# Optimization experiments

Hardware: AMD Instinct MI355X
Metric: run time of the kernel (lower is better)

Reference implementation:

```python
import jax, jax.numpy as jnp
import numpy as np

GROUPS = 8
EPS = 1e-5


def group_norm_dim1(x, gamma, beta):
    # Faithful to torch: GroupNorm treats dim 1 (height) as the channel axis.
    B, H, W, C = x.shape
    xg = x.reshape(B, GROUPS, H // GROUPS, W, C)
    mean = xg.mean(axis=(2, 3, 4), keepdims=True)
    var = xg.var(axis=(2, 3, 4), keepdims=True)
    xn = ((xg - mean) * jax.lax.rsqrt(var + EPS)).reshape(B, H, W, C)
    return xn * gamma[None, :, None, None] + beta[None, :, None, None]


def setup_inputs() -> dict:
    key = jax.random.key(0)
    ks = jax.random.split(key, 8)
    B, H, W, C = 4, 64, 64, 64  # height must equal units for GroupNorm to apply
    s = 1.0 / np.sqrt(C)
    return {
        "x": jax.random.normal(ks[0], (B, H, W, C), dtype=jnp.float32),
        "gamma": jnp.ones((C,), jnp.float32),
        "beta": jnp.zeros((C,), jnp.float32),
        "Wq": jax.random.normal(ks[1], (C, C), jnp.float32) * s,
        "bq": jnp.zeros((C,), jnp.float32),
        "Wk": jax.random.normal(ks[2], (C, C), jnp.float32) * s,
        "bk": jnp.zeros((C,), jnp.float32),
        "Wv": jax.random.normal(ks[3], (C, C), jnp.float32) * s,
        "bv": jnp.zeros((C,), jnp.float32),
        "Wo": jax.random.normal(ks[4], (C, C), jnp.float32) * s,
        "bo": jnp.zeros((C,), jnp.float32),
    }


def reference(x, gamma, beta, Wq, bq, Wk, bk, Wv, bv, Wo, bo):
    B, H, W, C = x.shape
    scale = C ** (-0.5)
    xn = group_norm_dim1(x, gamma, beta)
    q = xn @ Wq + bq
    k = xn @ Wk + bk
    v = xn @ Wv + bv
    # full spatial self-attention: scores [B, H, W, H*W]
    scores = jnp.einsum('bhwc,bijc->bhwij', q, k) * scale
    attn = jax.nn.softmax(scores.reshape(B, H, W, H * W), axis=-1)
    attn = attn.reshape(B, H, W, H, W)
    proj = jnp.einsum('bhwij,bijc->bhwc', attn, v)
    proj = proj @ Wo + bo
    return xn + proj
```

## Files before the change

### kernel.cpp

```cpp
#include <hip/hip_runtime.h>

typedef __bf16 bf16_t;
typedef bf16_t bf16x8 __attribute__((ext_vector_type(8)));
typedef bf16_t bf16x4 __attribute__((ext_vector_type(4)));
typedef short  short4v __attribute__((ext_vector_type(4)));
typedef float  f32x4  __attribute__((ext_vector_type(4)));

#define MFMA32(a, b, c) __builtin_amdgcn_mfma_f32_16x16x32_bf16(a, b, c, 0, 0, 0)
#define MFMA16(a, b, c) __builtin_amdgcn_mfma_f32_16x16x16bf16_1k(a, b, c, 0, 0, 0)

__global__ __launch_bounds__(256) void gn1w_kernel(const float* __restrict__ x,
    float2* __restrict__ partials,
    const float* __restrict__ Wq, const float* __restrict__ Wk,
    const float* __restrict__ Wv, const float* __restrict__ Wo,
    bf16_t* __restrict__ Wt) {
  int blk = blockIdx.x, t = threadIdx.x;
  if (blk >= 256) {
    int idx = (blk - 256) * 256 + t;
    int wsel = idx >> 12, rem = idx & 4095;
    int c = rem >> 6, kk = rem & 63;
    const float* src = (wsel == 0) ? Wq : ((wsel == 1) ? Wk : ((wsel == 2) ? Wv : Wo));
    Wt[idx] = (bf16_t)src[kk * 64 + c];
    return;
  }
  const float4* x4 = (const float4*)x + (size_t)blk * 1024;
  float s = 0.f, sq = 0.f;
  #pragma unroll
  for (int u = 0; u < 4; ++u) {
    float4 v = x4[u * 256 + t];
    s  += v.x + v.y + v.z + v.w;
    sq += v.x * v.x + v.y * v.y + v.z * v.z + v.w * v.w;
  }
  for (int off = 32; off; off >>= 1) {
    s  += __shfl_down(s, off, 64);
    sq += __shfl_down(sq, off, 64);
  }
  __shared__ float2 ps[4];
  if ((t & 63) == 0) ps[t >> 6] = make_float2(s, sq);
  __syncthreads();
  if (t == 0) {
    float S = 0.f, Q = 0.f;
    #pragma unroll
    for (int i = 0; i < 4; ++i) { S += ps[i].x; Q += ps[i].y; }
    partials[blk] = make_float2(S, Q);
  }
}

__global__ __launch_bounds__(256) void gnqkv_kernel(
    const float* __restrict__ x, const float* __restrict__ gamma,
    const float* __restrict__ beta, const float2* __restrict__ parts,
    const bf16_t* __restrict__ Wt,
    const float* __restrict__ bq, const float* __restrict__ bk, const float* __restrict__ bv,
    bf16_t* __restrict__ xnb, bf16_t* __restrict__ qo, bf16_t* __restrict__ ko,
    bf16_t* __restrict__ vo) {
  __shared__ __align__(16) bf16_t xl[4096];
  int blk = blockIdx.x, t = threadIdx.x;
  int grp = blk >> 3;
  float S = 0.f, Q = 0.f;
  #pragma unroll
  for (int i = 0; i < 8; ++i) { float2 p = parts[grp * 8 + i]; S += p.x; Q += p.y; }
  float mean = S * (1.f / 32768.f);
  float rstd = rsqrtf(Q * (1.f / 32768.f) - mean * mean + 1e-5f);
  int h = blk & 63;
  float ga = gamma[h] * rstd;
  float be = beta[h] - mean * ga;
  {
    int r = t >> 2, col0 = (t & 3) * 16;
    const float4* x4 = (const float4*)(x + (size_t)blk * 4096 + r * 64 + col0);
    bf16x8 pk0, pk1;
    float4 v0 = x4[0], v1 = x4[1], v2 = x4[2], v3 = x4[3];
    pk0[0] = (bf16_t)(v0.x * ga + be); pk0[1] = (bf16_t)(v0.y * ga + be);
    pk0[2] = (bf16_t)(v0.z * ga + be); pk0[3] = (bf16_t)(v0.w * ga + be);
    pk0[4] = (bf16_t)(v1.x * ga + be); pk0[5] = (bf16_t)(v1.y * ga + be);
    pk0[6] = (bf16_t)(v1.z * ga + be); pk0[7] = (bf16_t)(v1.w * ga + be);
    pk1[0] = (bf16_t)(v2.x * ga + be); pk1[1] = (bf16_t)(v2.y * ga + be);
    pk1[2] = (bf16_t)(v2.z * ga + be); pk1[3] = (bf16_t)(v2.w * ga + be);
    pk1[4] = (bf16_t)(v3.x * ga + be); pk1[5] = (bf16_t)(v3.y * ga + be);
    pk1[6] = (bf16_t)(v3.z * ga + be); pk1[7] = (bf16_t)(v3.w * ga + be);
    *(bf16x8*)&xnb[(size_t)blk * 4096 + r * 64 + col0]     = pk0;
    *(bf16x8*)&xnb[(size_t)blk * 4096 + r * 64 + col0 + 8] = pk1;
    int sw = r & 7, j0 = (t & 3) * 2;
    *(bf16x8*)&xl[r * 64 + ((j0 ^ sw) << 3)]       = pk0;
    *(bf16x8*)&xl[r * 64 + (((j0 + 1) ^ sw) << 3)] = pk1;
  }
  __syncthreads();
  int w = t >> 6, lane = t & 63, quad = lane >> 4, l16 = lane & 15;
  int rl = w * 16 + l16, sw2 = rl & 7;
  bf16x8 a0 = *(const bf16x8*)&xl[rl * 64 + ((quad ^ sw2) << 3)];
  bf16x8 a1 = *(const bf16x8*)&xl[rl * 64 + (((quad + 4) ^ sw2) << 3)];
  int m0 = blk * 64 + w * 16;
  int bi = m0 >> 12;
  f32x4 zero = {0.f, 0.f, 0.f, 0.f};
  const float QSCALE = 0.125f * 1.44269504088896340736f;
  #pragma unroll
  for (int outk = 0; outk < 3; ++outk) {
    const bf16_t* wt = Wt + outk * 4096;
    const float* bias = (outk == 0) ? bq : ((outk == 1) ? bk : bv);
    #pragma unroll
    for (int nt = 0; nt < 4; ++nt) {
      int col = nt * 16 + l16;
      bf16x8 b0 = *(const bf16x8*)&wt[col * 64 + quad * 8];
      bf16x8 b1 = *(const bf16x8*)&wt[col * 64 + 32 + quad * 8];
      f32x4 acc = MFMA32(a0, b0, zero);
      acc = MFMA32(a1, b1, acc);
      float bb = bias[col];
      if (outk == 2) {
        bf16x4 pk;
        #pragma unroll
        for (int r = 0; r < 4; ++r) pk[r] = (bf16_t)(acc[r] + bb);
        *(bf16x4*)&vo[(size_t)bi * 262144 + (size_t)(blk & 63) * 4096
                      + (size_t)col * 64 + w * 16 + quad * 4] = pk;
      } else {
        #pragma unroll
        for (int r = 0; r < 4; ++r) {
          int m = m0 + quad * 4 + r;
          float v = acc[r] + bb;
          if (outk == 0) qo[(size_t)m * 64 + col] = (bf16_t)(v * QSCALE);
          else           ko[(size_t)m * 64 + col] = (bf16_t)v;
        }
      }
    }
  }
}

__global__ __launch_bounds__(128) void flash_kernel(
    const bf16_t* __restrict__ q, const bf16_t* __restrict__ k,
    const bf16_t* __restrict__ vp, bf16_t* __restrict__ Opb, float* __restrict__ ml) {
  __shared__ __align__(16) bf16_t Kb[2][4096];
  __shared__ __align__(16) bf16_t Vb[2][4096];
  int t = threadIdx.x;
  int w = t >> 6, lane = t & 63, quad = lane >> 4, l16 = lane & 15;
  int qb = blockIdx.x, b = blockIdx.y, sp = blockIdx.z;
  int q0 = qb * 64 + w * 32;

  bf16x8 qf[2][2];
  {
    const bf16_t* qp = q + ((size_t)b * 4096 + q0 + l16) * 64;
    #pragma unroll
    for (int qt = 0; qt < 2; ++qt)
      #pragma unroll
      for (int hh = 0; hh < 2; ++hh)
        qf[qt][hh] = *(const bf16x8*)&qp[qt * 1024 + hh * 32 + quad * 8];
  }
  f32x4 o[2][4];
  f32x4 zero = {0.f, 0.f, 0.f, 0.f};
  #pragma unroll
  for (int qt = 0; qt < 2; ++qt)
    #pragma unroll
    for (int ct = 0; ct < 4; ++ct) o[qt][ct] = zero;
  float rs[2] = {0.f, 0.f};

  const bf16_t* kbase = k  + (size_t)b * 262144 + (size_t)sp * 131072;
  const bf16_t* vbase = vp + (size_t)b * 262144 + (size_t)sp * 131072;

  {
    bf16x8 ks[4], vs[4];
    #pragma unroll
    for (int i = 0; i < 4; ++i) {
      ks[i] = *(const bf16x8*)&kbase[i * 1024 + t * 8];
      vs[i] = *(const bf16x8*)&vbase[i * 1024 + t * 8];
    }
    #pragma unroll
    for (int i = 0; i < 4; ++i) {
      int e = i * 1024 + t * 8;
      int row = e >> 6;
      int ch = (e >> 3) & 7;
      *(bf16x8*)&Kb[0][row * 64 + ((ch ^ (row & 7)) << 3)] = ks[i];
      int u = (e >> 2) & 15;
      *(bf16x8*)&Vb[0][row * 64 + ((u ^ ((row & 7) << 1)) << 2)] = vs[i];
    }
  }
  __syncthreads();

  int swk = l16 & 7;
  int swv = (l16 & 7) << 1;

  for (int it = 0; it < 32; ++it) {
    int cur = it & 1;
    bf16x8 ks[4], vs[4];
    if (it < 31) {
      const bf16_t* kg = kbase + (it + 1) * 4096;
      const bf16_t* vg = vbase + (it + 1) * 4096;
      #pragma unroll
      for (int i = 0; i < 4; ++i) {
        ks[i] = *(const bf16x8*)&kg[i * 1024 + t * 8];
        vs[i] = *(const bf16x8*)&vg[i * 1024 + t * 8];
      }
    }
    const bf16_t* Kc = Kb[cur];
    const bf16_t* Vc = Vb[cur];
    #pragma unroll
    for (int kt = 0; kt < 4; ++kt) {
      int krow = (kt * 16 + l16) * 64;
      bf16x8 kf0 = *(const bf16x8*)&Kc[krow + ((quad ^ swk) << 3)];
      bf16x8 kf1 = *(const bf16x8*)&Kc[krow + (((quad + 4) ^ swk) << 3)];
      short4v va[4];
      #pragma unroll
      for (int ct = 0; ct < 4; ++ct)
        va[ct] = *(const short4v*)&Vc[(ct * 16 + l16) * 64 + (((kt * 4 + quad) ^ swv) << 2)];
      #pragma unroll
      for (int qt = 0; qt < 2; ++qt) {
        f32x4 st = MFMA32(kf0, qf[qt][0], zero);
        st = MFMA32(kf1, qf[qt][1], st);
        bf16x4 pb;
        float psum = 0.f;
        #pragma unroll
        for (int r = 0; r < 4; ++r) {
          float p = __builtin_amdgcn_exp2f(st[r]);
          psum += p;
          pb[r] = (bf16_t)p;
        }
        rs[qt] += psum;
        short4v pshort = __builtin_bit_cast(short4v, pb);
        #pragma unroll
        for (int ct = 0; ct < 4; ++ct)
          o[qt][ct] = MFMA16(va[ct], pshort, o[qt][ct]);
      }
    }
    if (it < 31) {
      int nxt = cur ^ 1;
      #pragma unroll
      for (int i = 0; i < 4; ++i) {
        int e = i * 1024 + t * 8;
        int row = e >> 6;
        int ch = (e >> 3) & 7;
        *(bf16x8*)&Kb[nxt][row * 64 + ((ch ^ (row & 7)) << 3)] = ks[i];
        int u = (e >> 2) & 15;
        *(bf16x8*)&Vb[nxt][row * 64 + ((u ^ ((row & 7) << 1)) << 2)] = vs[i];
      }
    }
    __syncthreads();
  }

  #pragma unroll
  for (int qt = 0; qt < 2; ++qt) {
    rs[qt] += __shfl_xor(rs[qt], 16, 64);
    rs[qt] += __shfl_xor(rs[qt], 32, 64);
  }
  size_t rbase = (size_t)sp * 16384 + (size_t)b * 4096 + q0;
  #pragma unroll
  for (int qt = 0; qt < 2; ++qt) {
    size_t row = rbase + qt * 16 + l16;
    if (quad == 0) ml[row] = rs[qt];
    #pragma unroll
    for (int ct = 0; ct < 4; ++ct) {
      bf16x4 pk;
      #pragma unroll
      for (int r = 0; r < 4; ++r) pk[r] = (bf16_t)o[qt][ct][r];
      *(bf16x4*)&Opb[row * 64 + ct * 16 + quad * 4] = pk;
    }
  }
}

__global__ __launch_bounds__(256) void proj_kernel(
    const bf16_t* __restrict__ Opb, const float* __restrict__ ml,
    const bf16_t* __restrict__ Wt, const float* __restrict__ bo,
    const bf16_t* __restrict__ xnb, float* __restrict__ out) {
  int t = threadIdx.x, w = t >> 6, lane = t & 63, quad = lane >> 4, l16 = lane & 15;
  int r0 = blockIdx.x * 64 + w * 16;
  float acc0[8], acc1[8];
  #pragma unroll
  for (int e = 0; e < 8; ++e) { acc0[e] = 0.f; acc1[e] = 0.f; }
  float lsum = 0.f;
  #pragma unroll
  for (int s = 0; s < 2; ++s) {
    size_t rr = (size_t)s * 16384 + r0 + l16;
    bf16x8 f0 = *(const bf16x8*)&Opb[rr * 64 + quad * 8];
    bf16x8 f1 = *(const bf16x8*)&Opb[rr * 64 + 32 + quad * 8];
    #pragma unroll
    for (int e = 0; e < 8; ++e) { acc0[e] += (float)f0[e]; acc1[e] += (float)f1[e]; }
    lsum += ml[rr];
  }
  float linv = 1.f / lsum;
  bf16x8 a0, a1;
  #pragma unroll
  for (int e = 0; e < 8; ++e) {
    a0[e] = (bf16_t)(acc0[e] * linv);
    a1[e] = (bf16_t)(acc1[e] * linv);
  }
  f32x4 zero = {0.f, 0.f, 0.f, 0.f};
  const bf16_t* wt = Wt + 3 * 4096;
  #pragma unroll
  for (int nt = 0; nt < 4; ++nt) {
    int col = nt * 16 + l16;
    bf16x8 b0 = *(const bf16x8*)&wt[col * 64 + quad * 8];
    bf16x8 b1 = *(const bf16x8*)&wt[col * 64 + 32 + quad * 8];
    f32x4 acc = MFMA32(a0, b0, zero);
    acc = MFMA32(a1, b1, acc);
    float bb = bo[col];
    #pragma unroll
    for (int r = 0; r < 4; ++r) {
      size_t m = (size_t)r0 + quad * 4 + r;
      out[m * 64 + col] = acc[r] + bb + (float)xnb[m * 64 + col];
    }
  }
}

extern "C" void kernel_launch(void* const* d_in, const int* in_sizes, int n_in,
                              void* d_out, int out_size, void* d_ws, size_t ws_size,
                              hipStream_t stream) {
  const float* x     = (const float*)d_in[0];
  const float* gamma = (const float*)d_in[1];
  const float* beta  = (const float*)d_in[2];
  const float* Wq    = (const float*)d_in[3];
  const float* bq    = (const float*)d_in[4];
  const float* Wk    = (const float*)d_in[5];
  const float* bk    = (const float*)d_in[6];
  const float* Wv    = (const float*)d_in[7];
  const float* bv    = (const float*)d_in[8];
  const float* Wo    = (const float*)d_in[9];
  const float* bo    = (const float*)d_in[10];
  float* out = (float*)d_out;

  char* ws = (char*)d_ws;
  bf16_t* xnb   = (bf16_t*)(ws + 0);
  bf16_t* qb    = (bf16_t*)(ws + (2u  << 20));
  bf16_t* kb    = (bf16_t*)(ws + (4u  << 20));
  bf16_t* vb    = (bf16_t*)(ws + (6u  << 20));
  bf16_t* Opb   = (bf16_t*)(ws + (8u  << 20));
  float*  ml    = (float*)(ws + (12u << 20));
  float2* parts = (float2*)(ws + (13u << 20));
  bf16_t* Wt    = (bf16_t*)(ws + (13u << 20) + 4096);

  hipLaunchKernelGGL(gn1w_kernel,  dim3(320),       dim3(256), 0, stream, x, parts, Wq, Wk, Wv, Wo, Wt);
  hipLaunchKernelGGL(gnqkv_kernel, dim3(256),       dim3(256), 0, stream, x, gamma, beta, parts, Wt, bq, bk, bv, xnb, qb, kb, vb);
  hipLaunchKernelGGL(flash_kernel, dim3(64, 4, 2),  dim3(128), 0, stream, qb, kb, vb, Opb, ml);
  hipLaunchKernelGGL(proj_kernel,  dim3(256),       dim3(256), 0, stream, Opb, ml, Wt, bo, xnb, out);
}
```

Measured before the change: 138.9 us.

## Pre-swizzle K/V in global memory, DMA them straight to LDS, split keys four ways

The QKV kernel now writes K and V in the exact swizzled tile layout the attention kernel uses in LDS. This lets the flash kernel use global_load_lds direct copies instead of loading into registers and then storing to LDS. The key range is split into 4 chunks instead of 2, which doubles the grid, and the grid is reordered so batch varies fastest. The projection kernel now reduces 4 partials. The aim is to cut register pressure and VALU/LDS store work in the main loop and to raise occupancy, at the cost of more partial-output traffic and a larger workspace.

Result: faster. 127.0 us (-8.6%).

```diff
diff --git a/kernel.cpp b/kernel.cpp
--- a/kernel.cpp
+++ b/kernel.cpp
@@ -8,6 +8,11 @@
 
 #define MFMA32(a, b, c) __builtin_amdgcn_mfma_f32_16x16x32_bf16(a, b, c, 0, 0, 0)
 #define MFMA16(a, b, c) __builtin_amdgcn_mfma_f32_16x16x16bf16_1k(a, b, c, 0, 0, 0)
+
+typedef __attribute__((address_space(3))) unsigned int       lds_u32;
+typedef __attribute__((address_space(1))) const unsigned int glb_u32c;
+#define DMA16(GP, LP) __builtin_amdgcn_global_load_lds((glb_u32c*)(const void*)(GP), \
+                                                       (lds_u32*)(void*)(LP), 16, 0, 0)
 
 __global__ __launch_bounds__(256) void gn1w_kernel(const float* __restrict__ x,
     float2* __restrict__ partials,
@@ -89,7 +94,9 @@
   bf16x8 a0 = *(const bf16x8*)&xl[rl * 64 + ((quad ^ sw2) << 3)];
   bf16x8 a1 = *(const bf16x8*)&xl[rl * 64 + (((quad + 4) ^ sw2) << 3)];
   int m0 = blk * 64 + w * 16;
-  int bi = m0 >> 12;
+  int bi = blk >> 6;
+  int tile = blk & 63;
+  size_t tbase = (size_t)bi * 262144 + (size_t)tile * 4096;
   f32x4 zero = {0.f, 0.f, 0.f, 0.f};
   const float QSCALE = 0.125f * 1.44269504088896340736f;
   #pragma unroll
@@ -104,20 +111,25 @@
       f32x4 acc = MFMA32(a0, b0, zero);
       acc = MFMA32(a1, b1, acc);
       float bb = bias[col];
-      if (outk == 2) {
-        bf16x4 pk;
-        #pragma unroll
-        for (int r = 0; r < 4; ++r) pk[r] = (bf16_t)(acc[r] + bb);
-        *(bf16x4*)&vo[(size_t)bi * 262144 + (size_t)(blk & 63) * 4096
-                      + (size_t)col * 64 + w * 16 + quad * 4] = pk;
-      } else {
+      if (outk == 0) {
         #pragma unroll
         for (int r = 0; r < 4; ++r) {
           int m = m0 + quad * 4 + r;
-          float v = acc[r] + bb;
-          if (outk == 0) qo[(size_t)m * 64 + col] = (bf16_t)(v * QSCALE);
-          else           ko[(size_t)m * 64 + col] = (bf16_t)v;
+          qo[(size_t)m * 64 + col] = (bf16_t)((acc[r] + bb) * QSCALE);
         }
+      } else if (outk == 1) {
+        #pragma unroll
+        for (int r = 0; r < 4; ++r) {
+          int kk = (m0 & 63) + quad * 4 + r;
+          ko[tbase + kk * 64 + ((((col >> 3) ^ (kk & 7)) << 3) | (col & 7))]
+              = (bf16_t)(acc[r] + bb);
+        }
+      } else {
+        bf16x4 pk;
+        #pragma unroll
+        for (int r = 0; r < 4; ++r) pk[r] = (bf16_t)(acc[r] + bb);
+        int u = w * 4 + quad;
+        *(bf16x4*)&vo[tbase + col * 64 + ((u ^ ((col & 7) << 1)) << 2)] = pk;
       }
     }
   }
@@ -130,7 +142,7 @@
   __shared__ __align__(16) bf16_t Vb[2][4096];
   int t = threadIdx.x;
   int w = t >> 6, lane = t & 63, quad = lane >> 4, l16 = lane & 15;
-  int qb = blockIdx.x, b = blockIdx.y, sp = blockIdx.z;
+  int b = blockIdx.x, qb = blockIdx.y, sp = blockIdx.z;
   int q0 = qb * 64 + w * 32;
 
   bf16x8 qf[2][2];
@@ -150,41 +162,29 @@
     for (int ct = 0; ct < 4; ++ct) o[qt][ct] = zero;
   float rs[2] = {0.f, 0.f};
 
-  const bf16_t* kbase = k  + (size_t)b * 262144 + (size_t)sp * 131072;
-  const bf16_t* vbase = vp + (size_t)b * 262144 + (size_t)sp * 131072;
-
-  {
-    bf16x8 ks[4], vs[4];
-    #pragma unroll
-    for (int i = 0; i < 4; ++i) {
-      ks[i] = *(const bf16x8*)&kbase[i * 1024 + t * 8];
-      vs[i] = *(const bf16x8*)&vbase[i * 1024 + t * 8];
-    }
-    #pragma unroll
-    for (int i = 0; i < 4; ++i) {
-      int e = i * 1024 + t * 8;
-      int row = e >> 6;
-      int ch = (e >> 3) & 7;
-      *(bf16x8*)&Kb[0][row * 64 + ((ch ^ (row & 7)) << 3)] = ks[i];
-      int u = (e >> 2) & 15;
-      *(bf16x8*)&Vb[0][row * 64 + ((u ^ ((row & 7) << 1)) << 2)] = vs[i];
-    }
+  const bf16_t* kimg = k  + (size_t)b * 262144 + (size_t)sp * 65536 + w * 2048 + lane * 8;
+  const bf16_t* vimg = vp + (size_t)b * 262144 + (size_t)sp * 65536 + w * 2048 + lane * 8;
+
+  #pragma unroll
+  for (int i = 0; i < 4; ++i) {
+    DMA16(kimg + i * 512, &Kb[0][w * 2048 + i * 512]);
+    DMA16(vimg + i * 512, &Vb[0][w * 2048 + i * 512]);
   }
   __syncthreads();
 
   int swk = l16 & 7;
   int swv = (l16 & 7) << 1;
 
-  for (int it = 0; it < 32; ++it) {
+  for (int it = 0; it < 16; ++it) {
     int cur = it & 1;
-    bf16x8 ks[4], vs[4];
-    if (it < 31) {
-      const bf16_t* kg = kbase + (it + 1) * 4096;
-      const bf16_t* vg = vbase + (it + 1) * 4096;
+    if (it < 15) {
+      const bf16_t* kg = kimg + (it + 1) * 4096;
+      const bf16_t* vg = vimg + (it + 1) * 4096;
+      int nxt = cur ^ 1;
       #pragma unroll
       for (int i = 0; i < 4; ++i) {
-        ks[i] = *(const bf16x8*)&kg[i * 1024 + t * 8];
-        vs[i] = *(const bf16x8*)&vg[i * 1024 + t * 8];
+        DMA16(kg + i * 512, &Kb[nxt][w * 2048 + i * 512]);
+        DMA16(vg + i * 512, &Vb[nxt][w * 2048 + i * 512]);
       }
     }
     const bf16_t* Kc = Kb[cur];
@@ -217,18 +217,6 @@
           o[qt][ct] = MFMA16(va[ct], pshort, o[qt][ct]);
       }
     }
-    if (it < 31) {
-      int nxt = cur ^ 1;
-      #pragma unroll
-      for (int i = 0; i < 4; ++i) {
-        int e = i * 1024 + t * 8;
-        int row = e >> 6;
-        int ch = (e >> 3) & 7;
-        *(bf16x8*)&Kb[nxt][row * 64 + ((ch ^ (row & 7)) << 3)] = ks[i];
-        int u = (e >> 2) & 15;
-        *(bf16x8*)&Vb[nxt][row * 64 + ((u ^ ((row & 7) << 1)) << 2)] = vs[i];
-      }
-    }
     __syncthreads();
   }
 
@@ -263,7 +251,7 @@
   for (int e = 0; e < 8; ++e) { acc0[e] = 0.f; acc1[e] = 0.f; }
   float lsum = 0.f;
   #pragma unroll
-  for (int s = 0; s < 2; ++s) {
+  for (int s = 0; s < 4; ++s) {
     size_t rr = (size_t)s * 16384 + r0 + l16;
     bf16x8 f0 = *(const bf16x8*)&Opb[rr * 64 + quad * 8];
     bf16x8 f1 = *(const bf16x8*)&Opb[rr * 64 + 32 + quad * 8];
@@ -318,12 +306,12 @@
   bf16_t* kb    = (bf16_t*)(ws + (4u  << 20));
   bf16_t* vb    = (bf16_t*)(ws + (6u  << 20));
   bf16_t* Opb   = (bf16_t*)(ws + (8u  << 20));
-  float*  ml    = (float*)(ws + (12u << 20));
-  float2* parts = (float2*)(ws + (13u << 20));
-  bf16_t* Wt    = (bf16_t*)(ws + (13u << 20) + 4096);
+  float*  ml    = (float*)(ws + (16u << 20));
+  float2* parts = (float2*)(ws + (17u << 20));
+  bf16_t* Wt    = (bf16_t*)(ws + (17u << 20) + 4096);
 
   hipLaunchKernelGGL(gn1w_kernel,  dim3(320),       dim3(256), 0, stream, x, parts, Wq, Wk, Wv, Wo, Wt);
   hipLaunchKernelGGL(gnqkv_kernel, dim3(256),       dim3(256), 0, stream, x, gamma, beta, parts, Wt, bq, bk, bv, xnb, qb, kb, vb);
-  hipLaunchKernelGGL(flash_kernel, dim3(64, 4, 2),  dim3(128), 0, stream, qb, kb, vb, Opb, ml);
+  hipLaunchKernelGGL(flash_kernel, dim3(4, 64, 4),  dim3(128), 0, stream, qb, kb, vb, Opb, ml);
   hipLaunchKernelGGL(proj_kernel,  dim3(256),       dim3(256), 0, stream, Opb, ml, Wt, bo, xnb, out);
 }
```
